# Performance work log

Hardware: AMD Instinct MI355X
Metric: run time of the kernel (lower is better)

The kernel has to match this reference:

```python
import jax, jax.numpy as jnp
import numpy as np


def _retain(o1, others, W, bias):
    # o1: (b, s, h); others: (b, 4, s, h); W: (h, h); bias: (1,)
    q = o1 @ W                                        # (b, s, h)
    scores = jnp.einsum('bih,bkjh->bijk', q, others) + bias[0]  # (b, s1, s2, 4)
    w = jax.nn.softmax(scores, axis=-1)               # softmax over the 4 options
    # weight[:, :, :, k] @ option_k summed over k
    return jnp.einsum('bijk,bkjh->bih', w, others)


def setup_inputs() -> dict:
    key = jax.random.key(0)
    ks = jax.random.split(key, 7)
    b, s, h = 32, 256, 1024
    opts = {f'option{i+1}': jax.random.normal(ks[i], (b, s, h), dtype=jnp.float32)
            for i in range(5)}
    W = 0.02 * jax.random.normal(ks[5], (h, h), dtype=jnp.float32)
    bias = 0.02 * jax.random.normal(ks[6], (1,), dtype=jnp.float32)
    return {**opts, 'W': W, 'bias': bias}


def reference(option1, option2, option3, option4, option5, W, bias):
    opts = [option1, option2, option3, option4, option5]
    total = None
    for i in range(5):
        others = jnp.stack([opts[j] for j in range(5) if j != i], axis=1)  # (b,4,s,h)
        r = _retain(opts[i], others, W, bias)
        total = r if total is None else total + r
    return total / 2.0
```

## Files before the change

kernel.cpp:

```cpp
#include <hip/hip_runtime.h>
#include <hip/hip_bf16.h>
#include <stdint.h>


#define BB 32
#define SS 256
#define HH 1024

typedef __attribute__((ext_vector_type(4))) float f32x4;
typedef __attribute__((ext_vector_type(8))) __bf16 bf16x8;
typedef __attribute__((ext_vector_type(4))) __bf16 bf16x4;

__device__ constexpr int PAIR(int i, int n) { return i * 4 + (n > i ? n - 1 : n); }

__device__ __forceinline__ void gload_lds16(const void* g, void* l) {
  __builtin_amdgcn_global_load_lds((const __attribute__((address_space(1))) void*)g,
                                   (__attribute__((address_space(3))) void*)l, 16, 0, 0);
}

__global__ void canary(float* out, float v) { out[0] = v; }

__global__ __launch_bounds__(256) void cast_all(
    const float* p0, const float* p1, const float* p2, const float* p3, const float* p4,
    __bf16* __restrict__ dst)
{
  int m = blockIdx.x >> 12;
  long off = ((long)(blockIdx.x & 4095) * 256 + threadIdx.x) * 8;
  const float* src = m == 0 ? p0 : m == 1 ? p1 : m == 2 ? p2 : m == 3 ? p3 : p4;
  float4 v0 = *(const float4*)(src + off);
  float4 v1 = *(const float4*)(src + off + 4);
  bf16x8 h;
  h[0] = (__bf16)v0.x; h[1] = (__bf16)v0.y; h[2] = (__bf16)v0.z; h[3] = (__bf16)v0.w;
  h[4] = (__bf16)v1.x; h[5] = (__bf16)v1.y; h[6] = (__bf16)v1.z; h[7] = (__bf16)v1.w;
  *(bf16x8*)(dst + (long)m * BB * SS * HH + off) = h;
}

__global__ __launch_bounds__(256) void cast_trW(const float* __restrict__ src,
                                                __bf16* __restrict__ dstT)
{
  __shared__ __bf16 tile[64][72];
  int ct = blockIdx.x & 15, rt = blockIdx.x >> 4;
  const float* s = src + (long)(rt * 64) * 1024 + ct * 64;
  int t = threadIdx.x;
#pragma unroll
  for (int p = 0; p < 4; p++) {
    int c = t + p * 256;
    int row = c >> 4, c4 = c & 15;
    float4 v = *(const float4*)(s + (long)row * 1024 + c4 * 4);
    bf16x4 h;
    h[0] = (__bf16)v.x; h[1] = (__bf16)v.y; h[2] = (__bf16)v.z; h[3] = (__bf16)v.w;
    *(bf16x4*)&tile[row][c4 * 4] = h;
  }
  __syncthreads();
#pragma unroll
  for (int p = 0; p < 4; p++) {
    int c = t + p * 256;
    int hr = c >> 4, s4 = c & 15;
    bf16x4 h;
    h[0] = tile[s4 * 4 + 0][hr];
    h[1] = tile[s4 * 4 + 1][hr];
    h[2] = tile[s4 * 4 + 2][hr];
    h[3] = tile[s4 * 4 + 3][hr];
    *(bf16x4*)(dstT + (long)(ct * 64 + hr) * 1024 + rt * 64 + s4 * 4) = h;
  }
}

__global__ __launch_bounds__(512, 2) void qgemm256(
    const __bf16* __restrict__ A, const __bf16* __restrict__ Bt, __bf16* __restrict__ C)
{
  __shared__ __align__(16) char ldsb[2 * 65536];
  int lin = blockIdx.x;
  int xcd = lin & 7, idx = lin >> 3;
  int rt = xcd * 20 + (idx >> 2), ct = idx & 3;
  int t = threadIdx.x, l = t & 63, w = t >> 6;
  int wr = w >> 2, wc = w & 3;
  f32x4 acc[8][4] = {};

  const char* gp[8];
  int dstp[8];
#pragma unroll
  for (int p = 0; p < 8; p++) {
    int c = t + 512 * (p & 3);
    int row = c >> 3;
    int sg = (c & 7) ^ (row & 7);
    if (p < 4) {
      gp[p] = (const char*)(A + (long)(rt * 256 + row) * 1024 + sg * 8);
      dstp[p] = w * 1024 + (p & 3) * 8192;
    } else {
      gp[p] = (const char*)(Bt + (long)(ct * 256 + row) * 1024 + sg * 8);
      dstp[p] = 32768 + w * 1024 + (p & 3) * 8192;
    }
  }

  int lr = l & 15, sl = l >> 4;
  int sx0 = (sl ^ (lr & 7)) * 16;
  int sx1 = ((4 | sl) ^ (lr & 7)) * 16;
  int arow = (wr * 128 + lr) * 128;
  int brow = 32768 + (wc * 64 + lr) * 128;

#define TILE(CUR, DOSTAGE)                                                             \
  {                                                                                    \
    const char* base = ldsb + (CUR) * 65536;                                           \
    char* sbase = ldsb + ((CUR) ^ 1) * 65536;                                          \
    bf16x8 bfr[4][2], af[2][2];                                                        \
    _Pragma("unroll") for (int j = 0; j < 4; j++) {                                    \
      bfr[j][0] = *(const bf16x8*)(base + brow + j * 2048 + sx0);                      \
      bfr[j][1] = *(const bf16x8*)(base + brow + j * 2048 + sx1);                      \
    }                                                                                  \
    _Pragma("unroll") for (int ph = 0; ph < 4; ph++) {                                 \
      if (DOSTAGE) {                                                                   \
        gload_lds16(gp[ph], sbase + dstp[ph]);                                         \
        gload_lds16(gp[ph + 4], sbase + dstp[ph + 4]);                                 \
      }                                                                                \
      _Pragma("unroll") for (int ii = 0; ii < 2; ii++) {                               \
        int i = ph * 2 + ii;                                                           \
        af[ii][0] = *(const bf16x8*)(base + arow + i * 2048 + sx0);                    \
        af[ii][1] = *(const bf16x8*)(base + arow + i * 2048 + sx1);                    \
      }                                                                                \
      __builtin_amdgcn_s_setprio(1);                                                   \
      _Pragma("unroll") for (int ii = 0; ii < 2; ii++)                                 \
        _Pragma("unroll") for (int j = 0; j < 4; j++) {                                \
          acc[ph * 2 + ii][j] = __builtin_amdgcn_mfma_f32_16x16x32_bf16(               \
              af[ii][0], bfr[j][0], acc[ph * 2 + ii][j], 0, 0, 0);                     \
          acc[ph * 2 + ii][j] = __builtin_amdgcn_mfma_f32_16x16x32_bf16(               \
              af[ii][1], bfr[j][1], acc[ph * 2 + ii][j], 0, 0, 0);                     \
        }                                                                              \
      __builtin_amdgcn_s_setprio(0);                                                   \
    }                                                                                  \
    if (DOSTAGE) {                                                                     \
      _Pragma("unroll") for (int p = 0; p < 8; p++) gp[p] += 128;                      \
    }                                                                                  \
  }

  {
#pragma unroll
    for (int p = 0; p < 8; p++) {
      gload_lds16(gp[p], ldsb + dstp[p]);
      gp[p] += 128;
    }
  }
  asm volatile("s_waitcnt vmcnt(0)" ::: "memory");
  __builtin_amdgcn_s_barrier();
  for (int tt = 0; tt < 15; tt++) {
    TILE(tt & 1, 1)
    asm volatile("s_waitcnt vmcnt(0)" ::: "memory");
    __builtin_amdgcn_s_barrier();
  }
  TILE(1, 0)
#undef TILE

#pragma unroll
  for (int i = 0; i < 8; i++) {
    long mrow = (long)rt * 256 + wr * 128 + i * 16 + (sl << 2);
#pragma unroll
    for (int j = 0; j < 4; j++) {
      int n = ct * 256 + wc * 64 + j * 16 + lr;
#pragma unroll
      for (int r = 0; r < 4; r++)
        C[(mrow + r) * 1024 + n] = (__bf16)acc[i][j][r];
    }
  }
}

__global__ __launch_bounds__(256, 2) void gram_b16(
    const __bf16* __restrict__ Q, const __bf16* __restrict__ O, __bf16* __restrict__ V)
{
  __shared__ __align__(16) char ldsb[3 * 20480];
  int bid = blockIdx.x;
  int xcd = bid & 7, idx = bid >> 3;
  int b = xcd * 4 + (idx >> 6);
  int rem = idx & 63;
  int s1t = rem >> 3, s2t = rem & 7;
  int t = threadIdx.x, l = t & 63, w = t >> 6;
  int pr = w >> 1, pc = w & 1;
  f32x4 acc[20] = {};

  long qrow0 = (long)b * SS + s1t * 32;
  long orow0 = (long)b * SS + s2t * 32;
  int slog = (l & 3) ^ ((l >> 3) & 3);
  const char* gp0; const char* gp1; const char* gp2; const char* gp3; const char* gp4;
#define GP_INIT(GP, P)                                                                \
  {                                                                                   \
    int g = 4 * (P) + w;                                                              \
    int isQ = g < 10;                                                                 \
    int gg = isQ ? g : g - 10;                                                        \
    long row = (long)(gg >> 1) * (BB * SS) + (isQ ? qrow0 : orow0) + (g & 1) * 16 +   \
               (l >> 2);                                                              \
    GP = (const char*)((isQ ? Q : O) + row * HH + slog * 8);                          \
  }
  GP_INIT(gp0, 0) GP_INIT(gp1, 1) GP_INIT(gp2, 2) GP_INIT(gp3, 3) GP_INIT(gp4, 4)
#undef GP_INIT
  int g0 = w, g1 = 4 + w, g2 = 8 + w, g3 = 12 + w, g4 = 16 + w;

#define STAGE(BB_)                                                      \
  {                                                                     \
    char* base = ldsb + (BB_) * 20480;                                  \
    gload_lds16(gp0, base + g0 * 1024); gp0 += 64;                      \
    gload_lds16(gp1, base + g1 * 1024); gp1 += 64;                      \
    gload_lds16(gp2, base + g2 * 1024); gp2 += 64;                      \
    gload_lds16(gp3, base + g3 * 1024); gp3 += 64;                      \
    gload_lds16(gp4, base + g4 * 1024); gp4 += 64;                      \
  }

  int lr = l & 15, sl = l >> 4;
  int swz = (sl ^ ((lr >> 1) & 3)) * 16;
  int qoff = (pr * 16 + lr) * 64 + swz;
  int ooff = 10240 + (pc * 16 + lr) * 64 + swz;

#define COMPUTE(BB_)                                                                   \
  {                                                                                    \
    const char* base = ldsb + (BB_) * 20480;                                           \
    bf16x8 qf[5], of[5];                                                               \
    _Pragma("unroll") for (int m = 0; m < 5; m++) {                                    \
      qf[m] = *(const bf16x8*)(base + m * 2048 + qoff);                                \
      of[m] = *(const bf16x8*)(base + m * 2048 + ooff);                                \
    }                                                                                  \
    __builtin_amdgcn_s_setprio(1);                                                     \
    _Pragma("unroll") for (int i = 0; i < 5; i++) {                                    \
      _Pragma("unroll") for (int n = 0; n < 5; n++) {                                  \
        if (n != i)                                                                    \
          acc[PAIR(i, n)] =                                                            \
              __builtin_amdgcn_mfma_f32_16x16x32_bf16(qf[i], of[n], acc[PAIR(i, n)],   \
                                                      0, 0, 0);                        \
      }                                                                                \
    }                                                                                  \
    __builtin_amdgcn_s_setprio(0);                                                     \
  }

#define STEP(CUR, STG)                                          \
  asm volatile("s_waitcnt vmcnt(5)" ::: "memory");              \
  __builtin_amdgcn_s_barrier();                                 \
  STAGE(STG);                                                   \
  COMPUTE(CUR);

  STAGE(0)
  STAGE(1)
  for (int it = 0; it < 10; it++) {
    STEP(0, 2)
    STEP(1, 0)
    STEP(2, 1)
  }
  asm volatile("s_waitcnt vmcnt(5)" ::: "memory");
  __builtin_amdgcn_s_barrier();
  COMPUTE(0)
  asm volatile("s_waitcnt vmcnt(0)" ::: "memory");
  __builtin_amdgcn_s_barrier();
  COMPUTE(1)
#undef STEP
#undef COMPUTE
#undef STAGE

  int s1g = s1t * 32 + pr * 16 + ((l >> 4) << 2);
  int s2g = s2t * 32 + pc * 16 + (l & 15);
#pragma unroll
  for (int r = 0; r < 4; r++) {
    float vacc[5] = {0.f, 0.f, 0.f, 0.f, 0.f};
#pragma unroll
    for (int i = 0; i < 5; i++) {
      float gg[5];
      float mx = -3.0e38f;
#pragma unroll
      for (int n = 0; n < 5; n++)
        if (n != i) { gg[n] = acc[PAIR(i, n)][r]; mx = fmaxf(mx, gg[n]); }
      float ee[5], ssum = 0.f;
#pragma unroll
      for (int n = 0; n < 5; n++)
        if (n != i) { ee[n] = __expf(gg[n] - mx); ssum += ee[n]; }
      float inv = 1.0f / ssum;
#pragma unroll
      for (int n = 0; n < 5; n++)
        if (n != i) vacc[n] += ee[n] * inv;
    }
#pragma unroll
    for (int n = 0; n < 5; n++)
      V[((long)(n * 32 + b) * 256 + s1g + r) * 256 + s2g] = (__bf16)vacc[n];
  }
}

__global__ __launch_bounds__(256) void pvgemm(
    const __bf16* __restrict__ Vb, const __bf16* __restrict__ Obf, float* __restrict__ out)
{
  __shared__ __bf16 smA[128][40];
  __shared__ __bf16 smB[128][40];
  int bid = blockIdx.x;
  int b = bid >> 4, s1t = (bid >> 3) & 1, ht = bid & 7;
  int t = threadIdx.x, l = t & 63, w = t >> 6;
  int wm = w >> 1, wn = w & 1;
  f32x4 acc[4][4] = {};
#pragma unroll
  for (int n = 0; n < 5; n++) {
    const __bf16* On = Obf + (long)n * BB * SS * HH;
    for (int st2 = 0; st2 < 8; st2++) {
      int s20 = st2 * 32;
#pragma unroll
      for (int p = 0; p < 2; p++) {
        int c = t + p * 256;
        int row = c >> 2, sl = c & 3;
        *(bf16x8*)&smA[row][sl * 8] =
            *(const bf16x8*)(Vb + (long)(n * BB + b) * SS * SS + (long)(s1t * 128 + row) * SS +
                             s20 + sl * 8);
      }
      {
        int h4 = (t & 31) * 4, s2q = (t >> 5) * 4;
        const __bf16* src = On + ((long)b * 256 + s20 + s2q) * 1024 + ht * 128 + h4;
        bf16x4 v0 = *(const bf16x4*)(src);
        bf16x4 v1 = *(const bf16x4*)(src + 1024);
        bf16x4 v2 = *(const bf16x4*)(src + 2048);
        bf16x4 v3 = *(const bf16x4*)(src + 3072);
        bf16x4 c0, c1, c2, c3;
        c0[0] = v0[0]; c0[1] = v1[0]; c0[2] = v2[0]; c0[3] = v3[0];
        c1[0] = v0[1]; c1[1] = v1[1]; c1[2] = v2[1]; c1[3] = v3[1];
        c2[0] = v0[2]; c2[1] = v1[2]; c2[2] = v2[2]; c2[3] = v3[2];
        c3[0] = v0[3]; c3[1] = v1[3]; c3[2] = v2[3]; c3[3] = v3[3];
        *(bf16x4*)&smB[h4 + 0][s2q] = c0;
        *(bf16x4*)&smB[h4 + 1][s2q] = c1;
        *(bf16x4*)&smB[h4 + 2][s2q] = c2;
        *(bf16x4*)&smB[h4 + 3][s2q] = c3;
      }
      __syncthreads();
      bf16x8 af[4], bfr[4];
      int sl = l >> 4, lr = l & 15;
#pragma unroll
      for (int i = 0; i < 4; i++) {
        af[i]  = *(const bf16x8*)&smA[wm * 64 + i * 16 + lr][sl * 8];
        bfr[i] = *(const bf16x8*)&smB[wn * 64 + i * 16 + lr][sl * 8];
      }
#pragma unroll
      for (int i = 0; i < 4; i++)
#pragma unroll
        for (int j = 0; j < 4; j++)
          acc[i][j] = __builtin_amdgcn_mfma_f32_16x16x32_bf16(af[i], bfr[j], acc[i][j], 0, 0, 0);
      __syncthreads();
    }
  }
#pragma unroll
  for (int i = 0; i < 4; i++) {
    int m = s1t * 128 + wm * 64 + i * 16 + ((l >> 4) << 2);
#pragma unroll
    for (int j = 0; j < 4; j++) {
      int n = ht * 128 + wn * 64 + j * 16 + (l & 15);
#pragma unroll
      for (int r = 0; r < 4; r++)
        out[(long)(b * SS + m + r) * HH + n] = 0.5f * acc[i][j][r];
    }
  }
}

extern "C" void kernel_launch(void* const* d_in, const int* in_sizes, int n_in,
                              void* d_out, int out_size, void* d_ws, size_t ws_size,
                              hipStream_t stream)
{
  const size_t SZ_W = (size_t)HH * HH * 2;
  const size_t SZ_Q = (size_t)5 * BB * SS * HH * 2;
  const size_t SZ_V = (size_t)5 * BB * SS * SS * 2;
  const size_t SZ_O = (size_t)5 * BB * SS * HH * 2;
  const size_t NEED = SZ_W + SZ_Q + SZ_V + SZ_O;
  if (ws_size < NEED) {
    canary<<<1, 1, 0, stream>>>((float*)d_out, (float)(ws_size >> 20));
    return;
  }
  char* ws = (char*)d_ws;
  __bf16* Wt  = (__bf16*)ws;
  __bf16* Qb  = (__bf16*)(ws + SZ_W);
  __bf16* Vb  = (__bf16*)(ws + SZ_W + SZ_Q);
  __bf16* Obf = (__bf16*)(ws + SZ_W + SZ_Q + SZ_V);
  const float* o0 = (const float*)d_in[0];
  const float* o1 = (const float*)d_in[1];
  const float* o2 = (const float*)d_in[2];
  const float* o3 = (const float*)d_in[3];
  const float* o4 = (const float*)d_in[4];

  cast_trW<<<256, 256, 0, stream>>>((const float*)d_in[5], Wt);
  cast_all<<<5 * 4096, 256, 0, stream>>>(o0, o1, o2, o3, o4, Obf);
  qgemm256<<<640, 512, 0, stream>>>(Obf, Wt, Qb);
  gram_b16<<<2048, 256, 0, stream>>>(Qb, Obf, Vb);
  pvgemm<<<512, 256, 0, stream>>>(Vb, Obf, (float*)d_out);
}
```

Baseline: 279.9 us.

## Enlarge gram kernel tile to 64x64 with 512 threads for more operand reuse

The Gram/softmax kernel moves from 32x32 (s1,s2) tiles with 256 threads to 64x64 tiles with 512 threads. Each wave now computes two 16-column output subtiles and reuses its Q fragments across both. Global-to-LDS traffic per output element is halved and the grid shrinks from 2048 to 512 blocks. In exchange, the doubled accumulators (160 VGPRs) raise register pressure and LDS use grows to 120KB per block, which lowers occupancy, and the smaller grid gives fewer blocks to spread across CUs.

```diff
diff --git a/kernel.cpp b/kernel.cpp
--- a/kernel.cpp
+++ b/kernel.cpp
@@ -162,66 +162,72 @@
   }
 }
 
-__global__ __launch_bounds__(256, 2) void gram_b16(
+__global__ __launch_bounds__(512, 2) void gram64(
     const __bf16* __restrict__ Q, const __bf16* __restrict__ O, __bf16* __restrict__ V)
 {
-  __shared__ __align__(16) char ldsb[3 * 20480];
+  __shared__ __align__(16) char ldsb[3 * 40960];
   int bid = blockIdx.x;
   int xcd = bid & 7, idx = bid >> 3;
-  int b = xcd * 4 + (idx >> 6);
-  int rem = idx & 63;
-  int s1t = rem >> 3, s2t = rem & 7;
+  int b = xcd * 4 + (idx >> 4);
+  int rem = idx & 15;
+  int s1t = rem >> 2, s2t = rem & 3;
   int t = threadIdx.x, l = t & 63, w = t >> 6;
-  int pr = w >> 1, pc = w & 1;
-  f32x4 acc[20] = {};
-
-  long qrow0 = (long)b * SS + s1t * 32;
-  long orow0 = (long)b * SS + s2t * 32;
-  int slog = (l & 3) ^ ((l >> 3) & 3);
-  const char* gp0; const char* gp1; const char* gp2; const char* gp3; const char* gp4;
-#define GP_INIT(GP, P)                                                                \
-  {                                                                                   \
-    int g = 4 * (P) + w;                                                              \
-    int isQ = g < 10;                                                                 \
-    int gg = isQ ? g : g - 10;                                                        \
-    long row = (long)(gg >> 1) * (BB * SS) + (isQ ? qrow0 : orow0) + (g & 1) * 16 +   \
-               (l >> 2);                                                              \
-    GP = (const char*)((isQ ? Q : O) + row * HH + slog * 8);                          \
-  }
-  GP_INIT(gp0, 0) GP_INIT(gp1, 1) GP_INIT(gp2, 2) GP_INIT(gp3, 3) GP_INIT(gp4, 4)
-#undef GP_INIT
-  int g0 = w, g1 = 4 + w, g2 = 8 + w, g3 = 12 + w, g4 = 16 + w;
-
-#define STAGE(BB_)                                                      \
+  int wr = w >> 1, wc = w & 1;
+  f32x4 acc[20][2] = {};
+
+  const char* gp[5];
+#pragma unroll
+  for (int p = 0; p < 5; p++) {
+    int c = t + 512 * p;
+    int isQ = c < 1280;
+    int cc = isQ ? c : c - 1280;
+    int m = cc >> 8, rr = (cc >> 2) & 63;
+    int sg = (cc & 3) ^ ((cc >> 3) & 3);
+    long row = (long)m * (BB * SS) + (long)b * SS + (isQ ? s1t : s2t) * 64 + rr;
+    gp[p] = (const char*)((isQ ? Q : O) + row * HH + sg * 8);
+  }
+  int dstb = (t & ~63) << 4;
+
+#define STAGE(BUF)                                                      \
   {                                                                     \
-    char* base = ldsb + (BB_) * 20480;                                  \
-    gload_lds16(gp0, base + g0 * 1024); gp0 += 64;                      \
-    gload_lds16(gp1, base + g1 * 1024); gp1 += 64;                      \
-    gload_lds16(gp2, base + g2 * 1024); gp2 += 64;                      \
-    gload_lds16(gp3, base + g3 * 1024); gp3 += 64;                      \
-    gload_lds16(gp4, base + g4 * 1024); gp4 += 64;                      \
+    char* base = ldsb + (BUF) * 40960 + dstb;                           \
+    _Pragma("unroll") for (int p = 0; p < 5; p++) {                     \
+      gload_lds16(gp[p], base + p * 8192);                              \
+      gp[p] += 64;                                                      \
+    }                                                                   \
   }
 
   int lr = l & 15, sl = l >> 4;
   int swz = (sl ^ ((lr >> 1) & 3)) * 16;
-  int qoff = (pr * 16 + lr) * 64 + swz;
-  int ooff = 10240 + (pc * 16 + lr) * 64 + swz;
-
-#define COMPUTE(BB_)                                                                   \
+  int qoff = (wr * 16 + lr) * 64 + swz;
+  int ooff0 = 20480 + (wc * 32 + lr) * 64 + swz;
+  int ooff1 = ooff0 + 1024;
+
+#define COMPUTE(BUF)                                                                   \
   {                                                                                    \
-    const char* base = ldsb + (BB_) * 20480;                                           \
+    const char* base = ldsb + (BUF) * 40960;                                           \
     bf16x8 qf[5], of[5];                                                               \
-    _Pragma("unroll") for (int m = 0; m < 5; m++) {                                    \
-      qf[m] = *(const bf16x8*)(base + m * 2048 + qoff);                                \
-      of[m] = *(const bf16x8*)(base + m * 2048 + ooff);                                \
-    }                                                                                  \
+    _Pragma("unroll") for (int m = 0; m < 5; m++)                                      \
+      qf[m] = *(const bf16x8*)(base + m * 4096 + qoff);                                \
+    _Pragma("unroll") for (int m = 0; m < 5; m++)                                      \
+      of[m] = *(const bf16x8*)(base + m * 4096 + ooff0);                               \
     __builtin_amdgcn_s_setprio(1);                                                     \
     _Pragma("unroll") for (int i = 0; i < 5; i++) {                                    \
       _Pragma("unroll") for (int n = 0; n < 5; n++) {                                  \
         if (n != i)                                                                    \
-          acc[PAIR(i, n)] =                                                            \
-              __builtin_amdgcn_mfma_f32_16x16x32_bf16(qf[i], of[n], acc[PAIR(i, n)],   \
-                                                      0, 0, 0);                        \
+          acc[PAIR(i, n)][0] = __builtin_amdgcn_mfma_f32_16x16x32_bf16(                \
+              qf[i], of[n], acc[PAIR(i, n)][0], 0, 0, 0);                              \
+      }                                                                                \
+    }                                                                                  \
+    __builtin_amdgcn_s_setprio(0);                                                     \
+    _Pragma("unroll") for (int m = 0; m < 5; m++)                                      \
+      of[m] = *(const bf16x8*)(base + m * 4096 + ooff1);                               \
+    __builtin_amdgcn_s_setprio(1);                                                     \
+    _Pragma("unroll") for (int i = 0; i < 5; i++) {                                    \
+      _Pragma("unroll") for (int n = 0; n < 5; n++) {                                  \
+        if (n != i)                                                                    \
+          acc[PAIR(i, n)][1] = __builtin_amdgcn_mfma_f32_16x16x32_bf16(                \
+              qf[i], of[n], acc[PAIR(i, n)][1], 0, 0, 0);                              \
       }                                                                                \
     }                                                                                  \
     __builtin_amdgcn_s_setprio(0);                                                     \
@@ -250,30 +256,34 @@
 #undef COMPUTE
 #undef STAGE
 
-  int s1g = s1t * 32 + pr * 16 + ((l >> 4) << 2);
-  int s2g = s2t * 32 + pc * 16 + (l & 15);
-#pragma unroll
-  for (int r = 0; r < 4; r++) {
-    float vacc[5] = {0.f, 0.f, 0.f, 0.f, 0.f};
-#pragma unroll
-    for (int i = 0; i < 5; i++) {
-      float gg[5];
-      float mx = -3.0e38f;
+  int s1b = s1t * 64 + wr * 16 + sl * 4;
+  int s2b = s2t * 64 + wc * 32 + lr;
+#pragma unroll
+  for (int h = 0; h < 2; h++) {
+#pragma unroll
+    for (int r = 0; r < 4; r++) {
+      float vacc[5] = {0.f, 0.f, 0.f, 0.f, 0.f};
+#pragma unroll
+      for (int i = 0; i < 5; i++) {
+        float gg[5];
+        float mx = -3.0e38f;
+#pragma unroll
+        for (int n = 0; n < 5; n++)
+          if (n != i) { gg[n] = acc[PAIR(i, n)][h][r]; mx = fmaxf(mx, gg[n]); }
+        float ee[5], ssum = 0.f;
+#pragma unroll
+        for (int n = 0; n < 5; n++)
+          if (n != i) { ee[n] = __expf(gg[n] - mx); ssum += ee[n]; }
+        float inv = 1.0f / ssum;
+#pragma unroll
+        for (int n = 0; n < 5; n++)
+          if (n != i) vacc[n] += ee[n] * inv;
+      }
+      int s1 = s1b + r, s2 = s2b + h * 16;
 #pragma unroll
       for (int n = 0; n < 5; n++)
-        if (n != i) { gg[n] = acc[PAIR(i, n)][r]; mx = fmaxf(mx, gg[n]); }
-      float ee[5], ssum = 0.f;
-#pragma unroll
-      for (int n = 0; n < 5; n++)
-        if (n != i) { ee[n] = __expf(gg[n] - mx); ssum += ee[n]; }
-      float inv = 1.0f / ssum;
-#pragma unroll
-      for (int n = 0; n < 5; n++)
-        if (n != i) vacc[n] += ee[n] * inv;
-    }
-#pragma unroll
-    for (int n = 0; n < 5; n++)
-      V[((long)(n * 32 + b) * 256 + s1g + r) * 256 + s2g] = (__bf16)vacc[n];
+        V[((long)(n * BB + b) * SS + s1) * SS + s2] = (__bf16)vacc[n];
+    }
   }
 }
 
@@ -373,6 +383,6 @@
   cast_trW<<<256, 256, 0, stream>>>((const float*)d_in[5], Wt);
   cast_all<<<5 * 4096, 256, 0, stream>>>(o0, o1, o2, o3, o4, Obf);
   qgemm256<<<640, 512, 0, stream>>>(Obf, Wt, Qb);
-  gram_b16<<<2048, 256, 0, stream>>>(Qb, Obf, Vb);
+  gram64<<<512, 512, 0, stream>>>(Qb, Obf, Vb);
   pvgemm<<<512, 256, 0, stream>>>(Vb, Obf, (float*)d_out);
 }
```

Result: faster. 262.6 us, median of 2 (-6.2%).
